# Optimization experiments

Hardware: AMD Instinct MI355X
Metric: run time of the kernel (lower is better)

## Reference

```python
import jax, jax.numpy as jnp
import numpy as np

C = 1152            # hidden_size
HEADS_LA = 36       # LiteLA heads = hidden_size // 32
HEADS_X = 16        # cross-attention heads
HID = int(C * 2.5)  # GLUMBConv hidden = 2880
B, N, M = 2, 4096, 300
EPS_LA = 1e-8
EPS_LN = 1e-6


def _ln(x):
    # LayerNorm without affine (adaLN-single style)
    mu = jnp.mean(x, -1, keepdims=True)
    var = jnp.mean((x - mu) ** 2, -1, keepdims=True)
    return (x - mu) * jax.lax.rsqrt(var + EPS_LN)


def _lite_la(x, qkv_w, proj_w, proj_b):
    b, n, c = x.shape
    d = c // HEADS_LA
    qkv = x @ qkv_w.T                       # (B,N,3C)
    q, k, v = jnp.split(qkv, 3, -1)
    r = lambda t: t.transpose(0, 2, 1).reshape(b, HEADS_LA, d, n)
    q = jax.nn.relu(r(q))
    k = jax.nn.relu(r(k))
    v = r(v)
    # pad v with a row of ones (PAD_VAL=1) for the normalizer
    v = jnp.concatenate([v, jnp.ones((b, HEADS_LA, 1, n), v.dtype)], 2)  # (B,h,d+1,N)
    vk = jnp.einsum('bhdn,bhen->bhde', v, k)    # (B,h,d+1,d)
    out = jnp.einsum('bhde,bhen->bhdn', vk, q)  # (B,h,d+1,N)
    out = out[:, :, :-1] / (out[:, :, -1:] + EPS_LA)
    out = out.reshape(b, c, n).transpose(0, 2, 1)
    return out @ proj_w.T + proj_b


def _cross(x, y, q_w, q_b, kv_w, kv_b, pw, pb):
    b, n, c = x.shape
    d = c // HEADS_X
    q = (x @ q_w.T + q_b).reshape(b, n, HEADS_X, d).transpose(0, 2, 1, 3)
    k, v = jnp.split(y @ kv_w.T + kv_b, 2, -1)
    k = k.reshape(b, -1, HEADS_X, d).transpose(0, 2, 1, 3)
    v = v.reshape(b, -1, HEADS_X, d).transpose(0, 2, 1, 3)
    scale = float(1.0 / np.sqrt(d))
    a = jax.nn.softmax(jnp.einsum('bhnd,bhmd->bhnm', q, k) * scale, -1)
    o = jnp.einsum('bhnm,bhmd->bhnd', a, v).transpose(0, 2, 1, 3).reshape(b, n, c)
    return o @ pw.T + pb


def _glumb(x, inv_w, inv_b, dw_w, dw_b, pw_w):
    b, n, c = x.shape
    H = W = int(np.sqrt(n))
    h = jax.nn.silu(x @ inv_w.T + inv_b)          # 1x1 inverted conv + silu, (B,N,2*HID)
    h = h.transpose(0, 2, 1).reshape(b, 2 * HID, H, W)
    h = jax.lax.conv_general_dilated(
        h, dw_w, (1, 1), 'SAME',
        feature_group_count=2 * HID,
        dimension_numbers=('NCHW', 'OIHW', 'NCHW'))
    h = h + dw_b[None, :, None, None]
    a, g = jnp.split(h, 2, 1)
    h = a * jax.nn.silu(g)                         # GLU
    h = h.reshape(b, HID, n).transpose(0, 2, 1)
    return h @ pw_w.T                              # 1x1 point conv, no bias/act


def setup_inputs() -> dict:
    key = jax.random.key(0)
    ks = jax.random.split(key, 12)
    p = lambda k, shp: (0.02 * jax.random.normal(k, shp)).astype(jnp.float32)
    z = lambda shp: jnp.zeros(shp, jnp.float32)
    return dict(
        x=jax.random.normal(ks[0], (B, N, C), jnp.float32),
        y=jax.random.normal(ks[1], (B, M, C), jnp.float32),
        t=jax.random.normal(ks[2], (B, 6, C), jnp.float32),
        sst=p(ks[3], (6, C)),
        qkv_w=p(ks[4], (3 * C, C)),
        aproj_w=p(ks[5], (C, C)), aproj_b=z((C,)),
        q_w=p(ks[6], (C, C)), q_b=z((C,)),
        kv_w=p(ks[7], (2 * C, C)), kv_b=z((2 * C,)),
        cproj_w=p(ks[8], (C, C)), cproj_b=z((C,)),
        inv_w=p(ks[9], (2 * HID, C)), inv_b=z((2 * HID,)),
        dw_w=p(ks[10], (2 * HID, 1, 3, 3)), dw_b=z((2 * HID,)),
        pw_w=p(ks[11], (C, HID)),
    )


def reference(x, y, t, sst, qkv_w, aproj_w, aproj_b, q_w, q_b, kv_w, kv_b,
              cproj_w, cproj_b, inv_w, inv_b, dw_w, dw_b, pw_w):
    m = sst[None] + t  # (B,6,C)
    sh_a, sc_a, g_a, sh_m, sc_m, g_m = [m[:, i:i + 1] for i in range(6)]
    x = x + g_a * _lite_la(_ln(x) * (1 + sc_a) + sh_a, qkv_w, aproj_w, aproj_b)
    x = x + _cross(x, y, q_w, q_b, kv_w, kv_b, cproj_w, cproj_b)
    x = x + g_m * _glumb(_ln(x) * (1 + sc_m) + sh_m, inv_w, inv_b, dw_w, dw_b, pw_w)
    return x
```

## Files before the change

kernel.cpp:

```cpp
#include <hip/hip_runtime.h>
#include <hip/hip_bf16.h>
#include <cstdint>
#include <cstddef>

#define CD    1152
#define NTOK  4096
#define MTOK  300
#define BSZ   2
#define HID2  5760
#define HIDD  2880
#define ROWS  (BSZ*NTOK)
#define KVROWS (BSZ*MTOK)

using bf16 = __hip_bfloat16;
typedef __bf16 bf16x8 __attribute__((ext_vector_type(8)));
typedef float f32x4 __attribute__((ext_vector_type(4)));

__device__ __forceinline__ float b2f(bf16 h) { return __bfloat162float(h); }
__device__ __forceinline__ bf16  f2b(float f) { return __float2bfloat16(f); }
__device__ __forceinline__ bf16x8 bz8() {
    bf16x8 v;
    #pragma unroll
    for (int j = 0; j < 8; ++j) v[j] = (__bf16)0.0f;
    return v;
}

__device__ __forceinline__ void gload16(const void* g, void* l) {
    __builtin_amdgcn_global_load_lds(
        (const __attribute__((address_space(1))) void*)g,
        (__attribute__((address_space(3))) void*)l, 16, 0, 0);
}

__global__ void cast_bf(const float* __restrict__ in, bf16* __restrict__ o, int n) {
    int i = blockIdx.x * 256 + threadIdx.x;
    if (i < n) o[i] = f2b(in[i]);
}

__global__ void zero_f32(float* __restrict__ p, int n) {
    int i = blockIdx.x * 256 + threadIdx.x;
    if (i < n) p[i] = 0.f;
}

__global__ void add_mod(const float* __restrict__ sst, const float* __restrict__ t,
                        float* __restrict__ m, int n, int per) {
    int i = blockIdx.x * 256 + threadIdx.x;
    if (i < n) m[i] = sst[i % per] + t[i];
}

__global__ void prep_dww(const float* __restrict__ dww, bf16* __restrict__ wt) {
    int i = blockIdx.x * 256 + threadIdx.x;
    if (i < 9 * HID2) {
        const int k = i / HID2, c = i - k * HID2;
        wt[i] = f2b(dww[c * 9 + k]);
    }
}

__global__ __launch_bounds__(256) void ln_mod(
    const float* __restrict__ xf, const float* __restrict__ m,
    int shRow, int scRow, bf16* __restrict__ out) {
    const int row = blockIdx.x;
    const int b = row >> 12;
    float s = 0.f, s2 = 0.f;
    for (int c = threadIdx.x; c < CD; c += 256) {
        float v = xf[(size_t)row * CD + c];
        s += v; s2 += v * v;
    }
    #pragma unroll
    for (int off = 32; off; off >>= 1) {
        s  += __shfl_down(s,  off, 64);
        s2 += __shfl_down(s2, off, 64);
    }
    __shared__ float red[8];
    const int wid = threadIdx.x >> 6, lane = threadIdx.x & 63;
    if (lane == 0) { red[wid] = s; red[4 + wid] = s2; }
    __syncthreads();
    s  = red[0] + red[1] + red[2] + red[3];
    s2 = red[4] + red[5] + red[6] + red[7];
    const float mu  = s / CD;
    const float var = s2 / CD - mu * mu;
    const float rs  = rsqrtf(var + 1e-6f);
    const float* sh = &m[((size_t)b * 6 + shRow) * CD];
    const float* sc = &m[((size_t)b * 6 + scRow) * CD];
    for (int c = threadIdx.x; c < CD; c += 256) {
        float v = xf[(size_t)row * CD + c];
        out[(size_t)row * CD + c] = f2b((v - mu) * rs * (1.f + sc[c]) + sh[c]);
    }
}

template<int EPI>
__global__ __launch_bounds__(256) void gemm_bt(
    const bf16* __restrict__ A, const bf16* __restrict__ W,
    const float* __restrict__ bias, const float* __restrict__ resf,
    const float* __restrict__ gate, int gateStride,
    bf16* __restrict__ outb, float* __restrict__ outf,
    int rows, int K, int Nout, int reluCols) {
    __shared__ bf16 As[128 * 32];
    __shared__ bf16 Bs[128 * 32];
    const int tid = threadIdx.x;
    const int row0 = blockIdx.x * 128;
    const int col0 = blockIdx.y * 128;
    const int wid = tid >> 6, lane = tid & 63;
    const int wm = wid & 1, wn = wid >> 1;
    const int l16 = lane & 15, l4 = lane >> 4;
    f32x4 acc[4][4] = {};

    const int r0 = tid >> 2;
    const int kb = (tid & 3) * 8;
    int gra0 = row0 + r0;      if (gra0 >= rows) gra0 = rows - 1;
    int gra1 = row0 + r0 + 64; if (gra1 >= rows) gra1 = rows - 1;
    const int gc0 = col0 + r0, gc1 = col0 + r0 + 64;

    char* AsB = (char*)As + wid * 1024;
    char* BsB = (char*)Bs + wid * 1024;

    for (int k0 = 0; k0 < K; k0 += 32) {
        __syncthreads();
        gload16(&A[(size_t)gra0 * K + k0 + kb], AsB);
        gload16(&A[(size_t)gra1 * K + k0 + kb], AsB + 4096);
        gload16(&W[(size_t)gc0 * K + k0 + kb], BsB);
        gload16(&W[(size_t)gc1 * K + k0 + kb], BsB + 4096);
        __syncthreads();
        bf16x8 a[4], b[4];
        #pragma unroll
        for (int i = 0; i < 4; ++i)
            a[i] = *(const bf16x8*)&As[(wm * 64 + i * 16 + l16) * 32 + l4 * 8];
        #pragma unroll
        for (int j = 0; j < 4; ++j)
            b[j] = *(const bf16x8*)&Bs[(wn * 64 + j * 16 + l16) * 32 + l4 * 8];
        #pragma unroll
        for (int i = 0; i < 4; ++i)
            #pragma unroll
            for (int j = 0; j < 4; ++j)
                acc[i][j] = __builtin_amdgcn_mfma_f32_16x16x32_bf16(a[i], b[j], acc[i][j], 0, 0, 0);
    }

    #pragma unroll
    for (int j = 0; j < 4; ++j) {
        const int gc = col0 + wn * 64 + j * 16 + l16;
        const float bv = (EPI != 1 && EPI != 5 && bias) ? bias[gc] : 0.0f;
        #pragma unroll
        for (int i = 0; i < 4; ++i) {
            #pragma unroll
            for (int r = 0; r < 4; ++r) {
                const int gr = row0 + wm * 64 + i * 16 + l4 * 4 + r;
                if (gr >= rows) continue;
                float v = acc[i][j][r];
                const size_t oi = (size_t)gr * Nout + gc;
                if (EPI == 0) { v += bv; outb[oi] = f2b(v); }
                else if (EPI == 1) { if (gc < reluCols) v = fmaxf(v, 0.0f); outb[oi] = f2b(v); }
                else if (EPI == 2) { v += bv; v = v / (1.0f + __expf(-v)); outb[oi] = f2b(v); }
                else if (EPI == 3) {
                    v += bv;
                    const int bb = gr >> 12;
                    v = resf[oi] + gate[bb * gateStride + gc] * v;
                    outf[oi] = v; outb[oi] = f2b(v);
                }
                else if (EPI == 4) { v += bv; outf[oi] = resf[oi] + v; }
                else if (EPI == 5) {
                    const int bb = gr >> 12;
                    outf[oi] = resf[oi] + gate[bb * gateStride + gc] * v;
                }
            }
        }
    }
}

__global__ __launch_bounds__(256) void lite_vk(
    const bf16* __restrict__ qkv, float* __restrict__ vk) {
    const int b = blockIdx.x / 36, h = blockIdx.x % 36;
    const int n0 = blockIdx.y * 256;
    __shared__ bf16 ksm[64 * 32];
    __shared__ bf16 vsm[64 * 32];
    const int t = threadIdx.x;
    const int ev = t >> 3, kq = (t & 7) * 4;
    float a0 = 0, a1 = 0, a2 = 0, a3 = 0;
    float q0 = 0, q1 = 0, q2 = 0, q3 = 0;
    for (int tile = 0; tile < 4; ++tile) {
        const int nb = n0 + tile * 64;
        __syncthreads();
        {
            const int nl = t >> 2, part = (t & 3) * 8;
            const size_t rbase = ((size_t)b * NTOK + nb + nl) * (3 * CD);
            *(bf16x8*)&ksm[nl * 32 + part] = *(const bf16x8*)&qkv[rbase + CD     + h * 32 + part];
            *(bf16x8*)&vsm[nl * 32 + part] = *(const bf16x8*)&qkv[rbase + 2 * CD + h * 32 + part];
        }
        __syncthreads();
        #pragma unroll 4
        for (int nl = 0; nl < 64; ++nl) {
            const float vv = b2f(vsm[nl * 32 + ev]);
            const float k0 = b2f(ksm[nl * 32 + kq + 0]);
            const float k1 = b2f(ksm[nl * 32 + kq + 1]);
            const float k2 = b2f(ksm[nl * 32 + kq + 2]);
            const float k3 = b2f(ksm[nl * 32 + kq + 3]);
            a0 += vv * k0; a1 += vv * k1; a2 += vv * k2; a3 += vv * k3;
            if (ev == 0) { q0 += k0; q1 += k1; q2 += k2; q3 += k3; }
        }
    }
    float* dst = &vk[(((size_t)b * 36 + h) * 33 + ev) * 32 + kq];
    atomicAdd(dst + 0, a0); atomicAdd(dst + 1, a1);
    atomicAdd(dst + 2, a2); atomicAdd(dst + 3, a3);
    if (ev == 0) {
        float* d2 = &vk[(((size_t)b * 36 + h) * 33 + 32) * 32 + kq];
        atomicAdd(d2 + 0, q0); atomicAdd(d2 + 1, q1);
        atomicAdd(d2 + 2, q2); atomicAdd(d2 + 3, q3);
    }
}

__global__ __launch_bounds__(256) void lite_out(
    const bf16* __restrict__ qkv, const float* __restrict__ vk,
    bf16* __restrict__ u) {
    const int b = blockIdx.x / 36, h = blockIdx.x % 36;
    const int n = blockIdx.y * 256 + threadIdx.x;
    __shared__ float vks[33 * 32];
    const float* src = &vk[((size_t)b * 36 + h) * 33 * 32];
    for (int i = threadIdx.x; i < 33 * 32; i += 256) vks[i] = src[i];
    __syncthreads();
    float q[32];
    const bf16* qp = &qkv[((size_t)b * NTOK + n) * (3 * CD) + h * 32];
    #pragma unroll
    for (int e = 0; e < 32; ++e) q[e] = b2f(qp[e]);
    float denom = 0.f;
    #pragma unroll
    for (int e = 0; e < 32; ++e) denom += vks[32 * 32 + e] * q[e];
    const float rd = 1.f / (denom + 1e-8f);
    bf16* up = &u[((size_t)b * NTOK + n) * CD + h * 32];
    #pragma unroll 1
    for (int d = 0; d < 32; ++d) {
        float acc = 0.f;
        #pragma unroll
        for (int e = 0; e < 32; ++e) acc += vks[d * 32 + e] * q[e];
        up[d] = f2b(acc * rd);
    }
}

__global__ __launch_bounds__(256) void cross_attn_mfma(
    const bf16* __restrict__ qx, const bf16* __restrict__ kvb,
    bf16* __restrict__ attn) {
    const int b = blockIdx.x >> 4, h = blockIdx.x & 15;
    const int row0 = blockIdx.y * 64;
    __shared__ bf16 Ks[320 * 72];
    __shared__ bf16 Vt[80 * 328];
    __shared__ bf16 Ps[64 * 328];
    const int tid = threadIdx.x;
    const int wid = tid >> 6, lane = tid & 63;
    const int l16 = lane & 15, l4 = lane >> 4;
    const bf16 zb = f2b(0.f);
    const bf16x8 zv8 = bz8();

    for (int i = tid; i < 80 * 328; i += 256) Vt[i] = zb;
    for (int idx = tid; idx < 320 * 9; idx += 256) {
        const int m = idx / 9, part = (idx % 9) * 8;
        if (m < MTOK)
            *(bf16x8*)&Ks[m * 72 + part] =
                *(const bf16x8*)&kvb[((size_t)b * MTOK + m) * (2 * CD) + h * 72 + part];
        else
            *(bf16x8*)&Ks[m * 72 + part] = zv8;
    }
    __syncthreads();
    for (int i = tid; i < MTOK * 72; i += 256) {
        const int m = i / 72, d = i - m * 72;
        Vt[d * 328 + m] = kvb[((size_t)b * MTOK + m) * (2 * CD) + CD + h * 72 + d];
    }
    for (int i = lane; i < 16 * 16; i += 64)
        Ps[(wid * 16 + (i >> 4)) * 328 + 304 + (i & 15)] = zb;

    bf16x8 aq[3];
    {
        const int qrow = row0 + wid * 16 + l16;
        const bf16* qp = &qx[((size_t)b * NTOK + qrow) * CD + h * 72];
        aq[0] = *(const bf16x8*)&qp[l4 * 8];
        aq[1] = *(const bf16x8*)&qp[32 + l4 * 8];
        aq[2] = (l4 == 0) ? *(const bf16x8*)&qp[64] : zv8;
    }

    f32x4 sa[19] = {};
    #pragma unroll
    for (int t = 0; t < 19; ++t) {
        const bf16* kr = &Ks[(t * 16 + l16) * 72];
        bf16x8 b0 = *(const bf16x8*)&kr[l4 * 8];
        bf16x8 b1 = *(const bf16x8*)&kr[32 + l4 * 8];
        bf16x8 b2 = (l4 == 0) ? *(const bf16x8*)&kr[64] : zv8;
        sa[t] = __builtin_amdgcn_mfma_f32_16x16x32_bf16(aq[0], b0, sa[t], 0, 0, 0);
        sa[t] = __builtin_amdgcn_mfma_f32_16x16x32_bf16(aq[1], b1, sa[t], 0, 0, 0);
        sa[t] = __builtin_amdgcn_mfma_f32_16x16x32_bf16(aq[2], b2, sa[t], 0, 0, 0);
    }

    const float scale = 0.11785113019775792f;
    if (l16 >= 12) { sa[18][0] = sa[18][1] = sa[18][2] = sa[18][3] = -3.0e37f; }
    float mr[4] = {-3.0e38f, -3.0e38f, -3.0e38f, -3.0e38f};
    #pragma unroll
    for (int t = 0; t < 19; ++t)
        #pragma unroll
        for (int r = 0; r < 4; ++r) {
            const float s = sa[t][r] * scale;
            sa[t][r] = s;
            mr[r] = fmaxf(mr[r], s);
        }
    #pragma unroll
    for (int off = 1; off < 16; off <<= 1)
        #pragma unroll
        for (int r = 0; r < 4; ++r)
            mr[r] = fmaxf(mr[r], __shfl_xor(mr[r], off, 64));
    float lr[4] = {0.f, 0.f, 0.f, 0.f};
    #pragma unroll
    for (int t = 0; t < 19; ++t)
        #pragma unroll
        for (int r = 0; r < 4; ++r) {
            const float p = __expf(sa[t][r] - mr[r]);
            lr[r] += p;
            Ps[(wid * 16 + l4 * 4 + r) * 328 + t * 16 + l16] = f2b(p);
        }
    #pragma unroll
    for (int off = 1; off < 16; off <<= 1)
        #pragma unroll
        for (int r = 0; r < 4; ++r)
            lr[r] += __shfl_xor(lr[r], off, 64);
    __syncthreads();

    f32x4 oa[5] = {};
    #pragma unroll
    for (int kc = 0; kc < 10; ++kc) {
        bf16x8 pa = *(const bf16x8*)&Ps[(wid * 16 + l16) * 328 + kc * 32 + l4 * 8];
        #pragma unroll
        for (int dt = 0; dt < 5; ++dt) {
            bf16x8 vb = *(const bf16x8*)&Vt[(dt * 16 + l16) * 328 + kc * 32 + l4 * 8];
            oa[dt] = __builtin_amdgcn_mfma_f32_16x16x32_bf16(pa, vb, oa[dt], 0, 0, 0);
        }
    }
    #pragma unroll
    for (int r = 0; r < 4; ++r) {
        const float rinv = 1.f / lr[r];
        const int gr = row0 + wid * 16 + l4 * 4 + r;
        bf16* op = &attn[((size_t)b * NTOK + gr) * CD + h * 72];
        #pragma unroll
        for (int dt = 0; dt < 5; ++dt) {
            const int d = dt * 16 + l16;
            if (d < 72) op[d] = f2b(oa[dt][r] * rinv);
        }
    }
}

__global__ __launch_bounds__(128) void dwconv_glu2(
    const bf16* __restrict__ hbuf, const bf16* __restrict__ wt,
    const float* __restrict__ dwb, bf16* __restrict__ glu) {
    const int cg = blockIdx.y * 128 + threadIdx.x;
    if (cg >= 360) return;
    const int c0 = cg * 8;
    const int n = blockIdx.x & 4095;
    const int b = blockIdx.x >> 12;
    const int y0 = n >> 6, x0 = n & 63;
    float a[8], g[8];
    #pragma unroll
    for (int j = 0; j < 8; ++j) { a[j] = dwb[c0 + j]; g[j] = dwb[HIDD + c0 + j]; }
    #pragma unroll
    for (int dy = -1; dy <= 1; ++dy) {
        const int yy = y0 + dy;
        if (yy < 0 || yy >= 64) continue;
        #pragma unroll
        for (int dx = -1; dx <= 1; ++dx) {
            const int xx = x0 + dx;
            if (xx < 0 || xx >= 64) continue;
            const int k = (dy + 1) * 3 + (dx + 1);
            const size_t base = ((size_t)b * NTOK + yy * 64 + xx) * HID2;
            const bf16x8 va = *(const bf16x8*)&hbuf[base + c0];
            const bf16x8 vg = *(const bf16x8*)&hbuf[base + HIDD + c0];
            const bf16x8 wa = *(const bf16x8*)&wt[k * HID2 + c0];
            const bf16x8 wg = *(const bf16x8*)&wt[k * HID2 + HIDD + c0];
            #pragma unroll
            for (int j = 0; j < 8; ++j) {
                a[j] += (float)wa[j] * (float)va[j];
                g[j] += (float)wg[j] * (float)vg[j];
            }
        }
    }
    bf16x8 o;
    #pragma unroll
    for (int j = 0; j < 8; ++j) {
        const float s = g[j] / (1.f + __expf(-g[j]));
        o[j] = (__bf16)(a[j] * s);
    }
    *(bf16x8*)&glu[((size_t)b * NTOK + n) * HIDD + c0] = o;
}

extern "C" void kernel_launch(void* const* d_in, const int* in_sizes, int n_in,
                              void* d_out, int out_size, void* d_ws, size_t ws_size,
                              hipStream_t stream) {
    (void)in_sizes; (void)n_in; (void)out_size; (void)ws_size;
    const float* x       = (const float*)d_in[0];
    const float* y       = (const float*)d_in[1];
    const float* t       = (const float*)d_in[2];
    const float* sst     = (const float*)d_in[3];
    const float* qkv_w   = (const float*)d_in[4];
    const float* aproj_w = (const float*)d_in[5];
    const float* aproj_b = (const float*)d_in[6];
    const float* q_w     = (const float*)d_in[7];
    const float* q_b     = (const float*)d_in[8];
    const float* kv_w    = (const float*)d_in[9];
    const float* kv_b    = (const float*)d_in[10];
    const float* cproj_w = (const float*)d_in[11];
    const float* cproj_b = (const float*)d_in[12];
    const float* inv_w   = (const float*)d_in[13];
    const float* inv_b   = (const float*)d_in[14];
    const float* dw_w    = (const float*)d_in[15];
    const float* dw_b    = (const float*)d_in[16];
    const float* pw_w    = (const float*)d_in[17];
    float* out = (float*)d_out;

    char* ws = (char*)d_ws;
    size_t cur = 0;
    auto take = [&](size_t bytes) -> char* {
        char* p = ws + cur;
        cur = (cur + bytes + 255) & ~(size_t)255;
        return p;
    };
    float* mbuf   = (float*)take(BSZ * 6 * CD * 4);
    float* vkbuf  = (float*)take(BSZ * 36 * 33 * 32 * 4);
    bf16* wqkv    = (bf16*)take((size_t)3 * CD * CD * 2);
    bf16* waproj  = (bf16*)take((size_t)CD * CD * 2);
    bf16* wq      = (bf16*)take((size_t)CD * CD * 2);
    bf16* wkv     = (bf16*)take((size_t)2 * CD * CD * 2);
    bf16* wcproj  = (bf16*)take((size_t)CD * CD * 2);
    bf16* winv    = (bf16*)take((size_t)HID2 * CD * 2);
    bf16* wpw     = (bf16*)take((size_t)CD * HIDD * 2);
    bf16* wtdw    = (bf16*)take((size_t)9 * HID2 * 2);
    bf16* yb      = (bf16*)take((size_t)KVROWS * CD * 2);
    bf16* kvbuf   = (bf16*)take((size_t)KVROWS * 2 * CD * 2);
    bf16* P       = (bf16*)take((size_t)ROWS * HID2 * 2);
    bf16* Q       = (bf16*)take((size_t)ROWS * HIDD * 2);
    bf16* R       = (bf16*)take((size_t)ROWS * CD * 2);
    bf16* S       = (bf16*)take((size_t)ROWS * CD * 2);
    float* xa_f   = (float*)take((size_t)ROWS * CD * 4);

    bf16* qkvb = P;  bf16* hbuf = P;
    bf16* ubuf = Q;  bf16* glub = Q;
    bf16* x1 = R, *xa_bf = R, *attnb = R, *x2 = R;
    bf16* qx = S;
    float* xb_f = out;

    auto cast = [&](const float* src, bf16* dst, int n) {
        cast_bf<<<(n + 255) / 256, 256, 0, stream>>>(src, dst, n);
    };

    add_mod<<<(BSZ * 6 * CD + 255) / 256, 256, 0, stream>>>(sst, t, mbuf, BSZ * 6 * CD, 6 * CD);
    cast(qkv_w,   wqkv,   3 * CD * CD);
    cast(aproj_w, waproj, CD * CD);
    cast(q_w,     wq,     CD * CD);
    cast(kv_w,    wkv,    2 * CD * CD);
    cast(cproj_w, wcproj, CD * CD);
    cast(inv_w,   winv,   HID2 * CD);
    cast(pw_w,    wpw,    CD * HIDD);
    cast(y,       yb,     KVROWS * CD);
    prep_dww<<<(9 * HID2 + 255) / 256, 256, 0, stream>>>(dw_w, wtdw);

    ln_mod<<<ROWS, 256, 0, stream>>>(x, mbuf, 0, 1, x1);
    gemm_bt<1><<<dim3(64, 27), 256, 0, stream>>>(x1, wqkv, nullptr, nullptr, nullptr, 0,
                                                 qkvb, nullptr, ROWS, CD, 3 * CD, 2 * CD);
    zero_f32<<<(BSZ * 36 * 33 * 32 + 255) / 256, 256, 0, stream>>>(vkbuf, BSZ * 36 * 33 * 32);
    lite_vk<<<dim3(72, 16), 256, 0, stream>>>(qkvb, vkbuf);
    lite_out<<<dim3(72, 16), 256, 0, stream>>>(qkvb, vkbuf, ubuf);
    gemm_bt<3><<<dim3(64, 9), 256, 0, stream>>>(ubuf, waproj, aproj_b, x, mbuf + 2 * CD, 6 * CD,
                                                xa_bf, xa_f, ROWS, CD, CD, 0);

    gemm_bt<0><<<dim3(64, 9), 256, 0, stream>>>(xa_bf, wq, q_b, nullptr, nullptr, 0,
                                                qx, nullptr, ROWS, CD, CD, 0);
    gemm_bt<0><<<dim3(5, 18), 256, 0, stream>>>(yb, wkv, kv_b, nullptr, nullptr, 0,
                                                kvbuf, nullptr, KVROWS, CD, 2 * CD, 0);
    cross_attn_mfma<<<dim3(32, 64), 256, 0, stream>>>(qx, kvbuf, attnb);
    gemm_bt<4><<<dim3(64, 9), 256, 0, stream>>>(attnb, wcproj, cproj_b, xa_f, nullptr, 0,
                                                nullptr, xb_f, ROWS, CD, CD, 0);

    ln_mod<<<ROWS, 256, 0, stream>>>(xb_f, mbuf, 3, 4, x2);
    gemm_bt<2><<<dim3(64, 45), 256, 0, stream>>>(x2, winv, inv_b, nullptr, nullptr, 0,
                                                 hbuf, nullptr, ROWS, CD, HID2, 0);
    dwconv_glu2<<<dim3(ROWS, 3), 128, 0, stream>>>(hbuf, wtdw, dw_b, glub);
    gemm_bt<5><<<dim3(64, 9), 256, 0, stream>>>(glub, wpw, nullptr, xb_f, mbuf + 5 * CD, 6 * CD,
                                                nullptr, out, ROWS, HIDD, CD, 0);
}
```

Baseline: 1.181 ms.

## Double GEMM K-tile with XOR-swizzled LDS and vectorized LDS-staged epilogue

The GEMM K step grows from 32 to 64. The LDS tiles are stored with an XOR swizzle to avoid bank conflicts when the MFMA fragments are read. The epilogue now stages the accumulators through shared memory in two passes, so each thread writes 8 contiguous outputs with vector stores instead of scattered scalar ones. This halves the number of barriers per K and makes global writes coalesced, at the cost of more LDS (33 KB), which may lower occupancy. The bias null checks are dropped, so the bias pointer must now be non-null for the epilogue modes that use it.

```diff
diff --git a/kernel.cpp b/kernel.cpp
--- a/kernel.cpp
+++ b/kernel.cpp
@@ -94,8 +94,9 @@
     const float* __restrict__ gate, int gateStride,
     bf16* __restrict__ outb, float* __restrict__ outf,
     int rows, int K, int Nout, int reluCols) {
-    __shared__ bf16 As[128 * 32];
-    __shared__ bf16 Bs[128 * 32];
+    __shared__ __align__(16) char smem[33792];
+    bf16* As = (bf16*)smem;
+    bf16* Bs = (bf16*)(smem + 16384);
     const int tid = threadIdx.x;
     const int row0 = blockIdx.x * 128;
     const int col0 = blockIdx.y * 128;
@@ -104,62 +105,133 @@
     const int l16 = lane & 15, l4 = lane >> 4;
     f32x4 acc[4][4] = {};
 
-    const int r0 = tid >> 2;
-    const int kb = (tid & 3) * 8;
-    int gra0 = row0 + r0;      if (gra0 >= rows) gra0 = rows - 1;
-    int gra1 = row0 + r0 + 64; if (gra1 >= rows) gra1 = rows - 1;
-    const int gc0 = col0 + r0, gc1 = col0 + r0 + 64;
-
-    char* AsB = (char*)As + wid * 1024;
-    char* BsB = (char*)Bs + wid * 1024;
-
-    for (int k0 = 0; k0 < K; k0 += 32) {
+    const int sr = tid >> 3;
+    const int kbsw = (((tid & 7) ^ (sr & 7)) << 3);
+    int gra[4], gcl[4];
+    #pragma unroll
+    for (int p = 0; p < 4; ++p) {
+        int r = row0 + p * 32 + sr; if (r >= rows) r = rows - 1;
+        gra[p] = r;
+        gcl[p] = col0 + p * 32 + sr;
+    }
+    char* AsB = smem + wid * 1024;
+    char* BsB = smem + 16384 + wid * 1024;
+
+    for (int k0 = 0; k0 < K; k0 += 64) {
         __syncthreads();
-        gload16(&A[(size_t)gra0 * K + k0 + kb], AsB);
-        gload16(&A[(size_t)gra1 * K + k0 + kb], AsB + 4096);
-        gload16(&W[(size_t)gc0 * K + k0 + kb], BsB);
-        gload16(&W[(size_t)gc1 * K + k0 + kb], BsB + 4096);
+        #pragma unroll
+        for (int p = 0; p < 4; ++p) {
+            gload16(&A[(size_t)gra[p] * K + k0 + kbsw], AsB + p * 4096);
+            gload16(&W[(size_t)gcl[p] * K + k0 + kbsw], BsB + p * 4096);
+        }
         __syncthreads();
-        bf16x8 a[4], b[4];
-        #pragma unroll
-        for (int i = 0; i < 4; ++i)
-            a[i] = *(const bf16x8*)&As[(wm * 64 + i * 16 + l16) * 32 + l4 * 8];
-        #pragma unroll
-        for (int j = 0; j < 4; ++j)
-            b[j] = *(const bf16x8*)&Bs[(wn * 64 + j * 16 + l16) * 32 + l4 * 8];
-        #pragma unroll
-        for (int i = 0; i < 4; ++i)
+        #pragma unroll
+        for (int kk = 0; kk < 2; ++kk) {
+            bf16x8 a[4], b[4];
             #pragma unroll
-            for (int j = 0; j < 4; ++j)
-                acc[i][j] = __builtin_amdgcn_mfma_f32_16x16x32_bf16(a[i], b[j], acc[i][j], 0, 0, 0);
-    }
-
-    #pragma unroll
-    for (int j = 0; j < 4; ++j) {
-        const int gc = col0 + wn * 64 + j * 16 + l16;
-        const float bv = (EPI != 1 && EPI != 5 && bias) ? bias[gc] : 0.0f;
-        #pragma unroll
-        for (int i = 0; i < 4; ++i) {
+            for (int i = 0; i < 4; ++i) {
+                const int ar = wm * 64 + i * 16 + l16;
+                a[i] = *(const bf16x8*)&As[ar * 64 + ((((kk << 2) + l4) ^ (ar & 7)) << 3)];
+            }
             #pragma unroll
-            for (int r = 0; r < 4; ++r) {
-                const int gr = row0 + wm * 64 + i * 16 + l4 * 4 + r;
-                if (gr >= rows) continue;
-                float v = acc[i][j][r];
-                const size_t oi = (size_t)gr * Nout + gc;
-                if (EPI == 0) { v += bv; outb[oi] = f2b(v); }
-                else if (EPI == 1) { if (gc < reluCols) v = fmaxf(v, 0.0f); outb[oi] = f2b(v); }
-                else if (EPI == 2) { v += bv; v = v / (1.0f + __expf(-v)); outb[oi] = f2b(v); }
-                else if (EPI == 3) {
-                    v += bv;
-                    const int bb = gr >> 12;
-                    v = resf[oi] + gate[bb * gateStride + gc] * v;
-                    outf[oi] = v; outb[oi] = f2b(v);
+            for (int j = 0; j < 4; ++j) {
+                const int br = wn * 64 + j * 16 + l16;
+                b[j] = *(const bf16x8*)&Bs[br * 64 + ((((kk << 2) + l4) ^ (br & 7)) << 3)];
+            }
+            #pragma unroll
+            for (int i = 0; i < 4; ++i)
+                #pragma unroll
+                for (int j = 0; j < 4; ++j)
+                    acc[i][j] = __builtin_amdgcn_mfma_f32_16x16x32_bf16(a[i], b[j], acc[i][j], 0, 0, 0);
+        }
+    }
+
+    float* Lf = (float*)smem;
+    const int erow = tid >> 4;
+    const int ecol = (tid & 15) * 8;
+    const int gc = col0 + ecol;
+    #pragma unroll
+    for (int pass = 0; pass < 2; ++pass) {
+        __syncthreads();
+        if (wm == pass) {
+            #pragma unroll
+            for (int i = 0; i < 4; ++i)
+                #pragma unroll
+                for (int j = 0; j < 4; ++j) {
+                    const int lc = wn * 64 + j * 16 + l16;
+                    #pragma unroll
+                    for (int r = 0; r < 4; ++r)
+                        Lf[(i * 16 + l4 * 4 + r) * 130 + lc] = acc[i][j][r];
                 }
-                else if (EPI == 4) { v += bv; outf[oi] = resf[oi] + v; }
-                else if (EPI == 5) {
-                    const int bb = gr >> 12;
-                    outf[oi] = resf[oi] + gate[bb * gateStride + gc] * v;
+        }
+        __syncthreads();
+        #pragma unroll
+        for (int rr = 0; rr < 4; ++rr) {
+            const int lrow = rr * 16 + erow;
+            const int gr = row0 + pass * 64 + lrow;
+            if (gr >= rows) continue;
+            float v[8];
+            #pragma unroll
+            for (int c = 0; c < 8; ++c) v[c] = Lf[lrow * 130 + ecol + c];
+            const size_t oi0 = (size_t)gr * Nout + gc;
+            if (EPI == 0) {
+                bf16x8 ob;
+                #pragma unroll
+                for (int c = 0; c < 8; ++c) ob[c] = (__bf16)(v[c] + bias[gc + c]);
+                *(bf16x8*)&outb[oi0] = ob;
+            } else if (EPI == 1) {
+                bf16x8 ob;
+                #pragma unroll
+                for (int c = 0; c < 8; ++c) {
+                    float t = v[c];
+                    if (gc + c < reluCols) t = fmaxf(t, 0.0f);
+                    ob[c] = (__bf16)t;
                 }
+                *(bf16x8*)&outb[oi0] = ob;
+            } else if (EPI == 2) {
+                bf16x8 ob;
+                #pragma unroll
+                for (int c = 0; c < 8; ++c) {
+                    float t = v[c] + bias[gc + c];
+                    t = t / (1.0f + __expf(-t));
+                    ob[c] = (__bf16)t;
+                }
+                *(bf16x8*)&outb[oi0] = ob;
+            } else if (EPI == 3) {
+                const float* gp = &gate[(gr >> 12) * gateStride + gc];
+                const float* rp = &resf[oi0];
+                f32x4 o0, o1; bf16x8 ob;
+                #pragma unroll
+                for (int c = 0; c < 8; ++c) {
+                    float t = v[c] + bias[gc + c];
+                    t = rp[c] + gp[c] * t;
+                    if (c < 4) o0[c] = t; else o1[c - 4] = t;
+                    ob[c] = (__bf16)t;
+                }
+                *(f32x4*)&outf[oi0] = o0;
+                *(f32x4*)&outf[oi0 + 4] = o1;
+                *(bf16x8*)&outb[oi0] = ob;
+            } else if (EPI == 4) {
+                const float* rp = &resf[oi0];
+                f32x4 o0, o1;
+                #pragma unroll
+                for (int c = 0; c < 8; ++c) {
+                    float t = rp[c] + v[c] + bias[gc + c];
+                    if (c < 4) o0[c] = t; else o1[c - 4] = t;
+                }
+                *(f32x4*)&outf[oi0] = o0;
+                *(f32x4*)&outf[oi0 + 4] = o1;
+            } else {
+                const float* gp = &gate[(gr >> 12) * gateStride + gc];
+                const float* rp = &resf[oi0];
+                f32x4 o0, o1;
+                #pragma unroll
+                for (int c = 0; c < 8; ++c) {
+                    float t = rp[c] + gp[c] * v[c];
+                    if (c < 4) o0[c] = t; else o1[c - 4] = t;
+                }
+                *(f32x4*)&outf[oi0] = o0;
+                *(f32x4*)&outf[oi0 + 4] = o1;
             }
         }
     }
```

New measurement: 1.185 ms. Within noise of the previous version (+0.3%).
